# Kernel tuning notes

Hardware: AMD Instinct MI355X
Metric: run time of the kernel (lower is better)

The kernel has to match this reference:

```python
import jax, jax.numpy as jnp
import numpy as np

D = 1024
H = 16
HD = D // H
B = 4
L = 2048
FFN = 4 * D
EPS = 1e-5


def _layer_norm(x, g, b):
    mu = jnp.mean(x, axis=-1, keepdims=True)
    var = jnp.mean(jnp.square(x - mu), axis=-1, keepdims=True)
    return (x - mu) * jax.lax.rsqrt(var + EPS) * g + b


def setup_inputs() -> dict:
    key = jax.random.key(0)
    ks = jax.random.split(key, 16)
    s = 1.0 / np.sqrt(D)
    inp = {
        "x": jax.random.normal(ks[0], (B, L, D), dtype=jnp.float32),
        "rel_pos_bias": jax.random.normal(ks[1], (1, H, L, L), dtype=jnp.float32) * 0.02,
        "wq": jax.random.normal(ks[2], (D, D), dtype=jnp.float32) * s,
        "bq": jnp.zeros((D,), jnp.float32),
        "wk": jax.random.normal(ks[3], (D, D), dtype=jnp.float32) * s,
        "bk": jnp.zeros((D,), jnp.float32),
        "wv": jax.random.normal(ks[4], (D, D), dtype=jnp.float32) * s,
        "bv": jnp.zeros((D,), jnp.float32),
        "wo": jax.random.normal(ks[5], (D, D), dtype=jnp.float32) * s,
        "bo": jnp.zeros((D,), jnp.float32),
        "g1": jnp.ones((D,), jnp.float32),
        "be1": jnp.zeros((D,), jnp.float32),
        "g2": jnp.ones((D,), jnp.float32),
        "be2": jnp.zeros((D,), jnp.float32),
        "w1": jax.random.normal(ks[6], (D, FFN), dtype=jnp.float32) * s,
        "bf1": jnp.zeros((FFN,), jnp.float32),
        "w2": jax.random.normal(ks[7], (FFN, D), dtype=jnp.float32) * (1.0 / np.sqrt(FFN)),
        "bf2": jnp.zeros((D,), jnp.float32),
    }
    return inp


def reference(x, rel_pos_bias, wq, bq, wk, bk, wv, bv, wo, bo,
              g1, be1, g2, be2, w1, bf1, w2, bf2):
    scale = HD ** -0.5
    residual = x
    xn = _layer_norm(x, g1, be1)
    # projections -> (B, H, L, HD)
    q = (xn @ wq + bq).reshape(B, L, H, HD).transpose(0, 2, 1, 3)
    k = (xn @ wk + bk).reshape(B, L, H, HD).transpose(0, 2, 1, 3)
    v = (xn @ wv + bv).reshape(B, L, H, HD).transpose(0, 2, 1, 3)
    scores = jnp.einsum('bhqd,bhkd->bhqk', q, k) * scale
    causal = jnp.tril(jnp.ones((L, L), dtype=bool))
    scores = jnp.where(causal[None, None], scores, -jnp.inf)
    scores = scores + rel_pos_bias
    attn = jax.nn.softmax(scores, axis=-1)
    out = jnp.einsum('bhqk,bhkd->bhqd', attn, v)
    out = out.transpose(0, 2, 1, 3).reshape(B, L, D)
    out = out @ wo + bo
    x = residual + out
    residual = x
    xn = _layer_norm(x, g2, be2)
    h = jax.nn.relu(xn @ w1 + bf1)
    x = residual + (h @ w2 + bf2)
    return x
```

## Files before the change

### kernel.cpp

```cpp
#include <hip/hip_runtime.h>
#include <hip/hip_bf16.h>

#define D_   1024
#define H_   16
#define HD_  64
#define B_   4
#define L_   2048
#define FFN_ 4096
#define M_   (B_ * L_)

typedef __bf16 bf16x8 __attribute__((ext_vector_type(8)));
typedef float f32x4 __attribute__((ext_vector_type(4)));
typedef unsigned short ushort8 __attribute__((ext_vector_type(8)));
typedef unsigned short ushort4v __attribute__((ext_vector_type(4)));

__device__ inline unsigned short f2bf(float f) {
    unsigned int u = __float_as_uint(f);
    u += 0x7fff + ((u >> 16) & 1);
    return (unsigned short)(u >> 16);
}
__device__ inline float bf2f(unsigned short u) {
    return __uint_as_float(((unsigned int)u) << 16);
}

__global__ __launch_bounds__(256) void k_transpose_bf16(
    const float* __restrict__ in, unsigned short* __restrict__ out, int K, int N)
{
    __shared__ float tile[64][65];
    int k0 = blockIdx.y * 64, n0 = blockIdx.x * 64;
    int t = threadIdx.x;
    int r = t >> 2, cs = (t & 3) * 16;
    const float* src = in + (size_t)(k0 + r) * N + n0 + cs;
#pragma unroll
    for (int i = 0; i < 16; i += 4) {
        float4 v = *(const float4*)(src + i);
        tile[r][cs + i + 0] = v.x;
        tile[r][cs + i + 1] = v.y;
        tile[r][cs + i + 2] = v.z;
        tile[r][cs + i + 3] = v.w;
    }
    __syncthreads();
    unsigned short* dst = out + (size_t)(n0 + r) * K + k0 + cs;
#pragma unroll
    for (int i = 0; i < 16; ++i) dst[i] = f2bf(tile[cs + i][r]);
}

__global__ void k_concat_bias(const float* __restrict__ bq, const float* __restrict__ bk,
                              const float* __restrict__ bv, float* __restrict__ out)
{
    int i = blockIdx.x * 256 + threadIdx.x;
    float v = (i < 1024) ? bq[i] : (i < 2048 ? bk[i - 1024] : bv[i - 2048]);
    out[i] = v;
}

__global__ __launch_bounds__(256) void k_layernorm(
    const float* __restrict__ x, const float* __restrict__ g, const float* __restrict__ be,
    unsigned short* __restrict__ out)
{
    int row = blockIdx.x;
    const float* xr = x + (size_t)row * D_;
    int t = threadIdx.x;
    float4 v = *(const float4*)(xr + t * 4);
    float s = v.x + v.y + v.z + v.w;
    float sq = v.x * v.x + v.y * v.y + v.z * v.z + v.w * v.w;
#pragma unroll
    for (int off = 32; off >= 1; off >>= 1) {
        s  += __shfl_down(s, off);
        sq += __shfl_down(sq, off);
    }
    __shared__ float ps[4], psq[4];
    int w = t >> 6;
    if ((t & 63) == 0) { ps[w] = s; psq[w] = sq; }
    __syncthreads();
    float tot  = ps[0] + ps[1] + ps[2] + ps[3];
    float totq = psq[0] + psq[1] + psq[2] + psq[3];
    float mu  = tot * (1.f / D_);
    float var = totq * (1.f / D_) - mu * mu;
    float inv = rsqrtf(var + 1e-5f);
    float4 gv = *(const float4*)(g + t * 4);
    float4 bv = *(const float4*)(be + t * 4);
    ushort4v o;
    o[0] = f2bf((v.x - mu) * inv * gv.x + bv.x);
    o[1] = f2bf((v.y - mu) * inv * gv.y + bv.y);
    o[2] = f2bf((v.z - mu) * inv * gv.z + bv.z);
    o[3] = f2bf((v.w - mu) * inv * gv.w + bv.w);
    *(ushort4v*)(out + (size_t)row * D_ + t * 4) = o;
}

template <bool OUT_BF16, bool RELU, bool RESID>
__global__ __launch_bounds__(256, 2) void k_gemm(
    const unsigned short* __restrict__ A, const unsigned short* __restrict__ Bt,
    const float* __restrict__ bias, const float* __restrict__ resid,
    void* __restrict__ Cout, int M, int N, int K)
{
    __shared__ unsigned short sA[128 * 40];
    __shared__ unsigned short sB[128 * 40];
    int m0 = blockIdx.y * 128, n0 = blockIdx.x * 128;
    int tid = threadIdx.x, lane = tid & 63, wvi = tid >> 6;
    int wm = (wvi & 1) * 64, wn = (wvi >> 1) * 64;
    int lr = lane & 15, qd = lane >> 4;

    f32x4 acc[4][4] = {};

    int sr = tid >> 2, ss = (tid & 3) * 8;
    const unsigned short* pA0 = A  + (size_t)(m0 + sr)      * K + ss;
    const unsigned short* pA1 = A  + (size_t)(m0 + 64 + sr) * K + ss;
    const unsigned short* pB0 = Bt + (size_t)(n0 + sr)      * K + ss;
    const unsigned short* pB1 = Bt + (size_t)(n0 + 64 + sr) * K + ss;

    for (int k0 = 0; k0 < K; k0 += 32) {
        ushort8 a0 = *(const ushort8*)(pA0 + k0);
        ushort8 a1 = *(const ushort8*)(pA1 + k0);
        ushort8 b0 = *(const ushort8*)(pB0 + k0);
        ushort8 b1 = *(const ushort8*)(pB1 + k0);
        if (k0) __syncthreads();
        *(ushort8*)(sA + sr * 40 + ss)        = a0;
        *(ushort8*)(sA + (64 + sr) * 40 + ss) = a1;
        *(ushort8*)(sB + sr * 40 + ss)        = b0;
        *(ushort8*)(sB + (64 + sr) * 40 + ss) = b1;
        __syncthreads();
        bf16x8 af[4], bfr[4];
#pragma unroll
        for (int i = 0; i < 4; ++i)
            af[i] = *(const bf16x8*)(sA + (wm + i * 16 + lr) * 40 + qd * 8);
#pragma unroll
        for (int i = 0; i < 4; ++i)
            bfr[i] = *(const bf16x8*)(sB + (wn + i * 16 + lr) * 40 + qd * 8);
#pragma unroll
        for (int mi = 0; mi < 4; ++mi)
#pragma unroll
            for (int ni = 0; ni < 4; ++ni)
                acc[mi][ni] = __builtin_amdgcn_mfma_f32_16x16x32_bf16(
                    af[mi], bfr[ni], acc[mi][ni], 0, 0, 0);
    }

#pragma unroll
    for (int ni = 0; ni < 4; ++ni) {
        int col = n0 + wn + ni * 16 + lr;
        float bvv = bias[col];
#pragma unroll
        for (int mi = 0; mi < 4; ++mi) {
#pragma unroll
            for (int r = 0; r < 4; ++r) {
                int row = m0 + wm + mi * 16 + qd * 4 + r;
                float v = acc[mi][ni][r] + bvv;
                if (RELU) v = fmaxf(v, 0.f);
                if (RESID) v += resid[(size_t)row * N + col];
                if (OUT_BF16)
                    ((unsigned short*)Cout)[(size_t)row * N + col] = f2bf(v);
                else
                    ((float*)Cout)[(size_t)row * N + col] = v;
            }
        }
    }
}

__global__ __launch_bounds__(256, 2) void k_attn(
    const unsigned short* __restrict__ qkv, const float* __restrict__ rpb,
    unsigned short* __restrict__ out)
{
    __shared__ unsigned short Qs[64 * 72];
    __shared__ unsigned short Ks[64 * 72];
    __shared__ unsigned short Vt[64 * 72];
    __shared__ unsigned short Sp[64 * 72];
    int h = blockIdx.x >> 2, b = blockIdx.x & 3;
    int q0 = blockIdx.y * 64;
    int t = threadIdx.x, lane = t & 63, w = t >> 6;
    int lr = lane & 15, qd = lane >> 4;
    int sr = t >> 2, ss = (t & 3) * 16;

    {
        const unsigned short* src = qkv + (size_t)(b * L_ + q0 + sr) * 3072 + h * 64 + ss;
        *(ushort8*)(Qs + sr * 72 + ss)     = *(const ushort8*)src;
        *(ushort8*)(Qs + sr * 72 + ss + 8) = *(const ushort8*)(src + 8);
    }

    f32x4 oacc[4] = {};
    float m_r[4], l_r[4];
#pragma unroll
    for (int r = 0; r < 4; ++r) { m_r[r] = -1e30f; l_r[r] = 0.f; }

    int ntile = q0 / 64 + 1;
    for (int kt = 0; kt < ntile; ++kt) {
        int k0 = kt * 64;
        __syncthreads();
        const unsigned short* ksrc = qkv + (size_t)(b * L_ + k0 + sr) * 3072 + 1024 + h * 64 + ss;
        *(ushort8*)(Ks + sr * 72 + ss)     = *(const ushort8*)ksrc;
        *(ushort8*)(Ks + sr * 72 + ss + 8) = *(const ushort8*)(ksrc + 8);
        const unsigned short* vsrc = qkv + (size_t)(b * L_ + k0 + sr) * 3072 + 2048 + h * 64 + ss;
        ushort8 v0 = *(const ushort8*)vsrc;
        ushort8 v1 = *(const ushort8*)(vsrc + 8);
#pragma unroll
        for (int i = 0; i < 8; ++i) Vt[(ss + i) * 72 + sr] = v0[i];
#pragma unroll
        for (int i = 0; i < 8; ++i) Vt[(ss + 8 + i) * 72 + sr] = v1[i];
        __syncthreads();

        f32x4 sc[4] = {};
#pragma unroll
        for (int ks = 0; ks < 2; ++ks) {
            bf16x8 aq = *(const bf16x8*)(Qs + (w * 16 + lr) * 72 + ks * 32 + qd * 8);
#pragma unroll
            for (int nt = 0; nt < 4; ++nt) {
                bf16x8 bk8 = *(const bf16x8*)(Ks + (nt * 16 + lr) * 72 + ks * 32 + qd * 8);
                sc[nt] = __builtin_amdgcn_mfma_f32_16x16x32_bf16(aq, bk8, sc[nt], 0, 0, 0);
            }
        }

        int qrow_base = q0 + w * 16 + qd * 4;
        const float* rpb_base = rpb + ((size_t)h * L_ + qrow_base) * L_ + k0;
        float pvv[4][4], mx[4];
#pragma unroll
        for (int r = 0; r < 4; ++r) {
            mx[r] = -1e30f;
#pragma unroll
            for (int nt = 0; nt < 4; ++nt) {
                int kcol = k0 + nt * 16 + lr;
                float sv = sc[nt][r] * 0.125f + rpb_base[(size_t)r * L_ + nt * 16 + lr];
                if (kcol > qrow_base + r) sv = -1e30f;
                pvv[r][nt] = sv;
                mx[r] = fmaxf(mx[r], sv);
            }
        }
#pragma unroll
        for (int r = 0; r < 4; ++r) {
            mx[r] = fmaxf(mx[r], __shfl_xor(mx[r], 1));
            mx[r] = fmaxf(mx[r], __shfl_xor(mx[r], 2));
            mx[r] = fmaxf(mx[r], __shfl_xor(mx[r], 4));
            mx[r] = fmaxf(mx[r], __shfl_xor(mx[r], 8));
        }
#pragma unroll
        for (int r = 0; r < 4; ++r) {
            float mnew  = fmaxf(m_r[r], mx[r]);
            float alpha = __expf(m_r[r] - mnew);
            float psum = 0.f;
#pragma unroll
            for (int nt = 0; nt < 4; ++nt) {
                float p = __expf(pvv[r][nt] - mnew);
                psum += p;
                Sp[(w * 16 + qd * 4 + r) * 72 + nt * 16 + lr] = f2bf(p);
            }
            psum += __shfl_xor(psum, 1);
            psum += __shfl_xor(psum, 2);
            psum += __shfl_xor(psum, 4);
            psum += __shfl_xor(psum, 8);
            l_r[r] = l_r[r] * alpha + psum;
            m_r[r] = mnew;
            oacc[0][r] *= alpha; oacc[1][r] *= alpha;
            oacc[2][r] *= alpha; oacc[3][r] *= alpha;
        }

#pragma unroll
        for (int ks = 0; ks < 2; ++ks) {
            bf16x8 ap = *(const bf16x8*)(Sp + (w * 16 + lr) * 72 + ks * 32 + qd * 8);
#pragma unroll
            for (int dt = 0; dt < 4; ++dt) {
                bf16x8 bv8 = *(const bf16x8*)(Vt + (dt * 16 + lr) * 72 + ks * 32 + qd * 8);
                oacc[dt] = __builtin_amdgcn_mfma_f32_16x16x32_bf16(ap, bv8, oacc[dt], 0, 0, 0);
            }
        }
    }

#pragma unroll
    for (int r = 0; r < 4; ++r) {
        float linv = 1.f / l_r[r];
        int qrow = q0 + w * 16 + qd * 4 + r;
        unsigned short* dst = out + (size_t)(b * L_ + qrow) * 1024 + h * 64;
#pragma unroll
        for (int dt = 0; dt < 4; ++dt)
            dst[dt * 16 + lr] = f2bf(oacc[dt][r] * linv);
    }
}

extern "C" void kernel_launch(void* const* d_in, const int* in_sizes, int n_in,
                              void* d_out, int out_size, void* d_ws, size_t ws_size,
                              hipStream_t stream)
{
    const float* x   = (const float*)d_in[0];
    const float* rpb = (const float*)d_in[1];
    const float* wq  = (const float*)d_in[2];
    const float* bq  = (const float*)d_in[3];
    const float* wk  = (const float*)d_in[4];
    const float* bk  = (const float*)d_in[5];
    const float* wv  = (const float*)d_in[6];
    const float* bv  = (const float*)d_in[7];
    const float* wo  = (const float*)d_in[8];
    const float* bo  = (const float*)d_in[9];
    const float* g1  = (const float*)d_in[10];
    const float* be1 = (const float*)d_in[11];
    const float* g2  = (const float*)d_in[12];
    const float* be2 = (const float*)d_in[13];
    const float* w1  = (const float*)d_in[14];
    const float* bf1 = (const float*)d_in[15];
    const float* w2  = (const float*)d_in[16];
    const float* bf2 = (const float*)d_in[17];
    float* out = (float*)d_out;
    char* ws = (char*)d_ws;

    unsigned short* xn1   = (unsigned short*)(ws + 0);
    unsigned short* qkv   = (unsigned short*)(ws + 16777216);
    unsigned short* attno = (unsigned short*)(ws + 0);
    unsigned short* hbuf  = (unsigned short*)(ws + 0);
    float*          xmid  = (float*)(ws + 67108864);
    unsigned short* xn2   = (unsigned short*)(ws + 100663296);
    unsigned short* wqkvT = (unsigned short*)(ws + 117440512);
    unsigned short* woT   = (unsigned short*)(ws + 123731968);
    unsigned short* w1T   = (unsigned short*)(ws + 125829120);
    unsigned short* w2T   = (unsigned short*)(ws + 134217728);
    float*          bqkv  = (float*)(ws + 142606336);

    k_transpose_bf16<<<dim3(16, 16), 256, 0, stream>>>(wq, wqkvT,                1024, 1024);
    k_transpose_bf16<<<dim3(16, 16), 256, 0, stream>>>(wk, wqkvT + 1024 * 1024,  1024, 1024);
    k_transpose_bf16<<<dim3(16, 16), 256, 0, stream>>>(wv, wqkvT + 2048 * 1024,  1024, 1024);
    k_transpose_bf16<<<dim3(16, 16), 256, 0, stream>>>(wo, woT,                  1024, 1024);
    k_transpose_bf16<<<dim3(64, 16), 256, 0, stream>>>(w1, w1T,                  1024, 4096);
    k_transpose_bf16<<<dim3(16, 64), 256, 0, stream>>>(w2, w2T,                  4096, 1024);
    k_concat_bias<<<12, 256, 0, stream>>>(bq, bk, bv, bqkv);

    k_layernorm<<<M_, 256, 0, stream>>>(x, g1, be1, xn1);
    k_gemm<true, false, false><<<dim3(24, 64), 256, 0, stream>>>(
        xn1, wqkvT, bqkv, nullptr, qkv, M_, 3072, 1024);
    k_attn<<<dim3(64, 32), 256, 0, stream>>>(qkv, rpb, attno);
    k_gemm<false, false, true><<<dim3(8, 64), 256, 0, stream>>>(
        attno, woT, bo, x, xmid, M_, 1024, 1024);
    k_layernorm<<<M_, 256, 0, stream>>>(xmid, g2, be2, xn2);
    k_gemm<true, true, false><<<dim3(32, 64), 256, 0, stream>>>(
        xn2, w1T, bf1, nullptr, hbuf, M_, 4096, 1024);
    k_gemm<false, false, true><<<dim3(8, 64), 256, 0, stream>>>(
        hbuf, w2T, bf2, xmid, out, M_, 1024, 4096);
}
```

Measured before the change: 1.024 ms.

## Restructure attention kernel: register prefetch, swizzled V transpose, heavy-first XCD-aware scheduling

```diff
diff --git a/kernel.cpp b/kernel.cpp
--- a/kernel.cpp
+++ b/kernel.cpp
@@ -155,24 +155,32 @@
     }
 }
 
-__global__ __launch_bounds__(256, 2) void k_attn(
+__global__ __launch_bounds__(256, 4) void k_attn(
     const unsigned short* __restrict__ qkv, const float* __restrict__ rpb,
     unsigned short* __restrict__ out)
 {
-    __shared__ unsigned short Qs[64 * 72];
     __shared__ unsigned short Ks[64 * 72];
-    __shared__ unsigned short Vt[64 * 72];
+    __shared__ unsigned short Vt[64 * 64];
     __shared__ unsigned short Sp[64 * 72];
-    int h = blockIdx.x >> 2, b = blockIdx.x & 3;
-    int q0 = blockIdx.y * 64;
+
+    int flat = blockIdx.x;
+    int xcd = flat & 7, b = (flat >> 3) & 3, hi = flat >> 5;
+    int g = hi * 8 + xcd;
+    int h = g & 15;
+    int qt = 31 - (g >> 4);
+    int q0 = qt * 64;
+
     int t = threadIdx.x, lane = t & 63, w = t >> 6;
     int lr = lane & 15, qd = lane >> 4;
     int sr = t >> 2, ss = (t & 3) * 16;
-
+    int bL = b * L_;
+
+    bf16x8 aq[2];
     {
-        const unsigned short* src = qkv + (size_t)(b * L_ + q0 + sr) * 3072 + h * 64 + ss;
-        *(ushort8*)(Qs + sr * 72 + ss)     = *(const ushort8*)src;
-        *(ushort8*)(Qs + sr * 72 + ss + 8) = *(const ushort8*)(src + 8);
+        const unsigned short* qsrc =
+            qkv + (size_t)(bL + q0 + w * 16 + lr) * 3072 + h * 64 + qd * 8;
+        aq[0] = *(const bf16x8*)qsrc;
+        aq[1] = *(const bf16x8*)(qsrc + 32);
     }
 
     f32x4 oacc[4] = {};
@@ -180,35 +188,67 @@
 #pragma unroll
     for (int r = 0; r < 4; ++r) { m_r[r] = -1e30f; l_r[r] = 0.f; }
 
-    int ntile = q0 / 64 + 1;
+    int qrow_base = q0 + w * 16 + qd * 4;
+    int ntile = qt + 1;
+
+    ushort8 krA, krB, vrA, vrB;
+    {
+        const unsigned short* kb_ = qkv + (size_t)(bL + sr) * 3072 + 1024 + h * 64 + ss;
+        krA = *(const ushort8*)kb_;  krB = *(const ushort8*)(kb_ + 8);
+        vrA = *(const ushort8*)(kb_ + 1024); vrB = *(const ushort8*)(kb_ + 1032);
+    }
+
     for (int kt = 0; kt < ntile; ++kt) {
         int k0 = kt * 64;
+        if (kt) __syncthreads();
+
+        *(ushort8*)(Ks + sr * 72 + ss)     = krA;
+        *(ushort8*)(Ks + sr * 72 + ss + 8) = krB;
+
+        {
+            int role = sr & 1;
+            int srp  = sr & ~1;
+#pragma unroll
+            for (int i = 0; i < 8; ++i) {
+                int sendv = role ? (int)(unsigned int)vrA[i] : (int)(unsigned int)vrB[i];
+                int got = __shfl_xor(sendv, 4);
+                int d = role ? (ss + 8 + i) : (ss + i);
+                unsigned short lo = role ? (unsigned short)got : vrA[i];
+                unsigned short hi = role ? vrB[i] : (unsigned short)got;
+                int swz = (d ^ (d >> 3)) & 7;
+                unsigned int u = (unsigned int)lo | ((unsigned int)hi << 16);
+                *(unsigned int*)(Vt + d * 64 + (srp ^ (swz << 3))) = u;
+            }
+        }
         __syncthreads();
-        const unsigned short* ksrc = qkv + (size_t)(b * L_ + k0 + sr) * 3072 + 1024 + h * 64 + ss;
-        *(ushort8*)(Ks + sr * 72 + ss)     = *(const ushort8*)ksrc;
-        *(ushort8*)(Ks + sr * 72 + ss + 8) = *(const ushort8*)(ksrc + 8);
-        const unsigned short* vsrc = qkv + (size_t)(b * L_ + k0 + sr) * 3072 + 2048 + h * 64 + ss;
-        ushort8 v0 = *(const ushort8*)vsrc;
-        ushort8 v1 = *(const ushort8*)(vsrc + 8);
-#pragma unroll
-        for (int i = 0; i < 8; ++i) Vt[(ss + i) * 72 + sr] = v0[i];
-#pragma unroll
-        for (int i = 0; i < 8; ++i) Vt[(ss + 8 + i) * 72 + sr] = v1[i];
-        __syncthreads();
-
-        f32x4 sc[4] = {};
+
+        float rv[4][4];
+        {
+            const float* rpb_base = rpb + ((size_t)h * L_ + qrow_base) * L_ + k0;
+#pragma unroll
+            for (int r = 0; r < 4; ++r)
+#pragma unroll
+                for (int nt = 0; nt < 4; ++nt)
+                    rv[r][nt] = rpb_base[(size_t)r * L_ + nt * 16 + lr];
+        }
+
+        if (kt + 1 < ntile) {
+            const unsigned short* kb_ =
+                qkv + (size_t)(bL + k0 + 64 + sr) * 3072 + 1024 + h * 64 + ss;
+            krA = *(const ushort8*)kb_;  krB = *(const ushort8*)(kb_ + 8);
+            vrA = *(const ushort8*)(kb_ + 1024); vrB = *(const ushort8*)(kb_ + 1032);
+        }
+
+        f32x4 sc4[4] = {};
 #pragma unroll
         for (int ks = 0; ks < 2; ++ks) {
-            bf16x8 aq = *(const bf16x8*)(Qs + (w * 16 + lr) * 72 + ks * 32 + qd * 8);
 #pragma unroll
             for (int nt = 0; nt < 4; ++nt) {
                 bf16x8 bk8 = *(const bf16x8*)(Ks + (nt * 16 + lr) * 72 + ks * 32 + qd * 8);
-                sc[nt] = __builtin_amdgcn_mfma_f32_16x16x32_bf16(aq, bk8, sc[nt], 0, 0, 0);
-            }
-        }
-
-        int qrow_base = q0 + w * 16 + qd * 4;
-        const float* rpb_base = rpb + ((size_t)h * L_ + qrow_base) * L_ + k0;
+                sc4[nt] = __builtin_amdgcn_mfma_f32_16x16x32_bf16(aq[ks], bk8, sc4[nt], 0, 0, 0);
+            }
+        }
+
         float pvv[4][4], mx[4];
 #pragma unroll
         for (int r = 0; r < 4; ++r) {
@@ -216,7 +256,7 @@
 #pragma unroll
             for (int nt = 0; nt < 4; ++nt) {
                 int kcol = k0 + nt * 16 + lr;
-                float sv = sc[nt][r] * 0.125f + rpb_base[(size_t)r * L_ + nt * 16 + lr];
+                float sv = sc4[nt][r] * 0.125f + rv[r][nt];
                 if (kcol > qrow_base + r) sv = -1e30f;
                 pvv[r][nt] = sv;
                 mx[r] = fmaxf(mx[r], sv);
@@ -255,7 +295,9 @@
             bf16x8 ap = *(const bf16x8*)(Sp + (w * 16 + lr) * 72 + ks * 32 + qd * 8);
 #pragma unroll
             for (int dt = 0; dt < 4; ++dt) {
-                bf16x8 bv8 = *(const bf16x8*)(Vt + (dt * 16 + lr) * 72 + ks * 32 + qd * 8);
+                int d = dt * 16 + lr;
+                int swz = (d ^ (d >> 3)) & 7;
+                bf16x8 bv8 = *(const bf16x8*)(Vt + d * 64 + ((ks * 32 + qd * 8) ^ (swz << 3)));
                 oacc[dt] = __builtin_amdgcn_mfma_f32_16x16x32_bf16(ap, bv8, oacc[dt], 0, 0, 0);
             }
         }
@@ -265,7 +307,7 @@
     for (int r = 0; r < 4; ++r) {
         float linv = 1.f / l_r[r];
         int qrow = q0 + w * 16 + qd * 4 + r;
-        unsigned short* dst = out + (size_t)(b * L_ + qrow) * 1024 + h * 64;
+        unsigned short* dst = out + (size_t)(bL + qrow) * 1024 + h * 64;
 #pragma unroll
         for (int dt = 0; dt < 4; ++dt)
             dst[dt * 16 + lr] = f2bf(oacc[dt][r] * linv);
@@ -320,7 +362,7 @@
     k_layernorm<<<M_, 256, 0, stream>>>(x, g1, be1, xn1);
     k_gemm<true, false, false><<<dim3(24, 64), 256, 0, stream>>>(
         xn1, wqkvT, bqkv, nullptr, qkv, M_, 3072, 1024);
-    k_attn<<<dim3(64, 32), 256, 0, stream>>>(qkv, rpb, attno);
+    k_attn<<<dim3(2048), 256, 0, stream>>>(qkv, rpb, attno);
     k_gemm<false, false, true><<<dim3(8, 64), 256, 0, stream>>>(
         attno, woT, bo, x, xmid, M_, 1024, 1024);
     k_layernorm<<<M_, 256, 0, stream>>>(xmid, g2, be2, xn2);
```

New measurement: 864.5 us. -15.6%, faster.
